# Performance work log

Measured on AMD Instinct MI355X. Metric: run time of the kernel, lower is better.

## Reference

```python
import jax, jax.numpy as jnp
import numpy as np

RADIUS = 4
SIGMA1 = 5.0
SIGMA2 = 1.0


def _gauss_1d(radius, sigma):
    x = jnp.arange(-radius, radius + 1, dtype=jnp.float32)
    return jnp.exp(-(x ** 2) / (2.0 * sigma ** 2))  # peak-1 gaussian (norm.pdf(d)/norm.pdf(0))


def _blur3d(x, g, radius):
    # Separable 3D gaussian conv; product of 1D kernels == exp(-(dx^2+dy^2+dz^2)/(2*sigma^2)),
    # mathematically identical to the dense (2r+1)^3 conv3d in the torch module.
    dn = ('NCDHW', 'OIDHW', 'NCDHW')
    for ax in range(3):
        shape = [1, 1, 1, 1, 1]
        shape[2 + ax] = g.shape[0]
        k = g.reshape(shape)
        pad = [(0, 0), (0, 0), (0, 0)]
        pad[ax] = (radius, radius)
        x = jax.lax.conv_general_dilated(x, k, (1, 1, 1), pad, dimension_numbers=dn)
    return x


def setup_inputs() -> dict:
    key = jax.random.key(0)
    k1, k2 = jax.random.split(key)
    labels = jax.random.uniform(k1, (2, 4, 128, 128, 128), dtype=jnp.float32)
    inputs = jax.random.normal(k2, (2, 1, 128, 128, 128), dtype=jnp.float32)
    return {"labels": labels, "inputs": inputs}


def reference(labels, inputs):
    num_classes = labels.shape[1]
    g = _gauss_1d(RADIUS, SIGMA1)
    loss = jnp.float32(0.0)
    for k in range(num_classes):
        class_probs = labels[:, k:k + 1]  # [B,1,D,H,W]
        class_mean = (jnp.mean(inputs * class_probs, axis=(2, 3, 4), keepdims=True)
                      / (jnp.mean(class_probs, axis=(2, 3, 4), keepdims=True) + 1e-5))  # [B,C,1,1,1]
        diff = jnp.sum((inputs - class_mean) ** 2, axis=1, keepdims=True)  # [B,1,D,H,W]
        weights = jnp.exp(-(diff ** 2) / (SIGMA2 ** 2))
        numerator = jnp.sum(class_probs * _blur3d(class_probs * weights, g, RADIUS))
        denominator = jnp.sum(class_probs * _blur3d(weights, g, RADIUS))
        # L1Loss(x, 0) on a scalar == |x|
        loss = loss + jnp.abs(numerator / (denominator + 1e-6))
    return num_classes - loss
```

## Files before the change

### kernel.cpp

```cpp
#include <hip/hip_runtime.h>
#include <math.h>

#define DIM   128
#define SLICE (DIM*DIM)
#define VOL   (DIM*DIM*DIM)
#define NK    4
#define NVOL  8
#define SSTR  33

__constant__ float c_g[9] = {
    0.72614904f, 0.83527021f, 0.92311635f, 0.98019867f, 1.0f,
    0.98019867f, 0.92311635f, 0.83527021f, 0.72614904f
};


__global__ __launch_bounds__(256) void k_sums(
    const float* __restrict__ labels, const float* __restrict__ inputs,
    float* __restrict__ red)
{
    const int b     = blockIdx.x >> 9;
    const int chunk = blockIdx.x & 511;
    const int t     = threadIdx.x;
    const size_t off4 = (size_t)chunk*1024 + t;
    const float4* __restrict__ I4 = (const float4*)inputs + (size_t)b*(VOL/4) + off4;
    const float4* __restrict__ L4 = (const float4*)labels;
    float sp[4] = {0,0,0,0}, sip[4] = {0,0,0,0};
    #pragma unroll
    for (int j = 0; j < 4; ++j) {
        const float4 iv = I4[j*256];
        #pragma unroll
        for (int k = 0; k < 4; ++k) {
            const float4 p = L4[(size_t)(b*NK + k)*(VOL/4) + off4 + j*256];
            sp[k]  += p.x + p.y + p.z + p.w;
            sip[k] += p.x*iv.x + p.y*iv.y + p.z*iv.z + p.w*iv.w;
        }
    }
    #pragma unroll
    for (int k = 0; k < 4; ++k) {
        #pragma unroll
        for (int o = 32; o; o >>= 1) {
            sp[k]  += __shfl_down(sp[k],  o);
            sip[k] += __shfl_down(sip[k], o);
        }
    }
    __shared__ float sB[8][4];
    const int wid = t >> 6;
    if ((t & 63) == 0) {
        #pragma unroll
        for (int k = 0; k < 4; ++k) { sB[k][wid] = sp[k]; sB[4+k][wid] = sip[k]; }
    }
    __syncthreads();
    if (t < 8) {
        const float v = sB[t][0] + sB[t][1] + sB[t][2] + sB[t][3];
        atomicAdd(&red[(t < 4 ? 0 : 8) + b*NK + (t & 3)], v);
    }
}

__global__ __launch_bounds__(256) void k_fused(
    const float* __restrict__ labels, const float* __restrict__ inputs,
    const float* __restrict__ red, float* __restrict__ nd)
{
    __shared__ float4 sW[2][16*SSTR + 8];
    __shared__ float sN[4], sD[4];

    const int dq    = blockIdx.x & 3;
    const int strip = (blockIdx.x >> 2) & 15;
    const int vol   = blockIdx.x >> 6;
    const int b = vol >> 2, kcls = vol & 3;
    const int d0 = dq * 32;
    const int t  = threadIdx.x;
    const float g1 = c_g[5], g2 = c_g[6], g3 = c_g[7], g4 = c_g[8];
    const float4 z4 = make_float4(0.f, 0.f, 0.f, 0.f);

    const float* __restrict__ src = labels + (size_t)vol*VOL;
    const float mean = red[8+vol] / (red[vol] + 20.97152f);

    const int r0 = t >> 5, c0 = t & 31;
    const int r1 = r0 + 8;
    const int ho = t >> 5, wq = t & 31;

    const int hA = strip*8 - 4 + r0;
    const int hB = strip*8 - 4 + r1;
    const bool vA = (unsigned)hA < 128u;
    const bool vB = (unsigned)hB < 128u;
    const float4* __restrict__ rowA = (const float4*)(src + (size_t)(vA ? hA : 0)*DIM);
    const float4* __restrict__ rowB = (const float4*)(src + (size_t)(vB ? hB : 0)*DIM);

    const size_t ob4 = (size_t)(strip*8 + ho)*(DIM/4) + wq;
    const float4* __restrict__ P4 = (const float4*)src + ob4;
    const float4* __restrict__ I4 = (const float4*)(inputs + (size_t)b*VOL) + ob4;

    float4 ring[9];
    #pragma unroll
    for (int i = 0; i < 9; ++i) ring[i] = z4;
    float numAcc = 0.f, denAcc = 0.f;

    auto ldA = [&](int s, float4& pv, float4& cv, float4& nx) {
        pv = cv = nx = z4;
        if (vA && (unsigned)s < 128u) {
            const float4* rp = rowA + (size_t)s*(SLICE/4);
            cv = rp[c0];
            if (c0 > 0)  pv = rp[c0-1];
            if (c0 < 31) nx = rp[c0+1];
        }
    };
    auto ldB = [&](int s, float4& pv, float4& cv, float4& nx) {
        pv = cv = nx = z4;
        if (vB && (unsigned)s < 128u) {
            const float4* rp = rowB + (size_t)s*(SLICE/4);
            cv = rp[c0];
            if (c0 > 0)  pv = rp[c0-1];
            if (c0 < 31) nx = rp[c0+1];
        }
    };

    float4 Apv, Acv, Anx, Bpv, Bcv, Bnx;
    ldA(d0-4, Apv, Acv, Anx);
    ldB(d0-4, Bpv, Bcv, Bnx);

    #pragma unroll 2
    for (int s = d0-4; s < d0+36; ++s) {
        const float4 apv=Apv, acv=Acv, anx=Anx, bpv=Bpv, bcv=Bcv, bnx=Bnx;
        ldA(s+1, Apv, Acv, Anx);
        ldB(s+1, Bpv, Bcv, Bnx);
        float4 pc = z4, ic = z4;
        const bool outStep = (s >= d0+4);
        if (outStep) {
            pc = P4[(size_t)(s-4)*(SLICE/4)];
            ic = I4[(size_t)(s-4)*(SLICE/4)];
        }
        const int buf = s & 1;
        {
            float4 o;
            o.x = acv.x + g1*(apv.w+acv.y) + g2*(apv.z+acv.z) + g3*(apv.y+acv.w) + g4*(apv.x+anx.x);
            o.y = acv.y + g1*(acv.x+acv.z) + g2*(apv.w+acv.w) + g3*(apv.z+anx.x) + g4*(apv.y+anx.y);
            o.z = acv.z + g1*(acv.y+acv.w) + g2*(acv.x+anx.x) + g3*(apv.w+anx.y) + g4*(apv.z+anx.z);
            o.w = acv.w + g1*(acv.z+anx.x) + g2*(acv.y+anx.y) + g3*(acv.x+anx.z) + g4*(apv.w+anx.w);
            sW[buf][r0*SSTR + c0] = o;
        }
        {
            float4 o;
            o.x = bcv.x + g1*(bpv.w+bcv.y) + g2*(bpv.z+bcv.z) + g3*(bpv.y+bcv.w) + g4*(bpv.x+bnx.x);
            o.y = bcv.y + g1*(bcv.x+bcv.z) + g2*(bpv.w+bcv.w) + g3*(bpv.z+bnx.x) + g4*(bpv.y+bnx.y);
            o.z = bcv.z + g1*(bcv.y+bcv.w) + g2*(bcv.x+bnx.x) + g3*(bpv.w+bnx.y) + g4*(bpv.z+bnx.z);
            o.w = bcv.w + g1*(bcv.z+bnx.x) + g2*(bcv.y+bnx.y) + g3*(bcv.x+bnx.z) + g4*(bpv.w+bnx.w);
            sW[buf][r1*SSTR + c0] = o;
        }
        __syncthreads();
        float4 acc = sW[buf][(ho+4)*SSTR + wq];
        #pragma unroll
        for (int dt = 1; dt <= 4; ++dt) {
            const float g = c_g[4+dt];
            const float4 u = sW[buf][(ho+4-dt)*SSTR + wq];
            const float4 v = sW[buf][(ho+4+dt)*SSTR + wq];
            acc.x += g*(u.x+v.x); acc.y += g*(u.y+v.y);
            acc.z += g*(u.z+v.z); acc.w += g*(u.w+v.w);
        }
        #pragma unroll
        for (int i = 0; i < 8; ++i) ring[i] = ring[i+1];
        ring[8] = acc;
        if (outStep) {
            float4 B = ring[4];
            #pragma unroll
            for (int dt = 1; dt <= 4; ++dt) {
                const float g = c_g[4+dt];
                B.x += g*(ring[4+dt].x + ring[4-dt].x);
                B.y += g*(ring[4+dt].y + ring[4-dt].y);
                B.z += g*(ring[4+dt].z + ring[4-dt].z);
                B.w += g*(ring[4+dt].w + ring[4-dt].w);
            }
            { float df = ic.x - mean; df *= df; const float bw = B.x * __expf(-df*df); numAcc += bw*pc.x; denAcc += bw; }
            { float df = ic.y - mean; df *= df; const float bw = B.y * __expf(-df*df); numAcc += bw*pc.y; denAcc += bw; }
            { float df = ic.z - mean; df *= df; const float bw = B.z * __expf(-df*df); numAcc += bw*pc.z; denAcc += bw; }
            { float df = ic.w - mean; df *= df; const float bw = B.w * __expf(-df*df); numAcc += bw*pc.w; denAcc += bw; }
        }
    }

    #pragma unroll
    for (int o = 32; o; o >>= 1) { numAcc += __shfl_down(numAcc, o); denAcc += __shfl_down(denAcc, o); }
    if ((t & 63) == 0) { sN[t >> 6] = numAcc; sD[t >> 6] = denAcc; }
    __syncthreads();
    if (t == 0) {
        atomicAdd(&nd[kcls],   sN[0]+sN[1]+sN[2]+sN[3]);
        atomicAdd(&nd[4+kcls], sD[0]+sD[1]+sD[2]+sD[3]);
    }
}

__global__ void k_final(const float* __restrict__ red, float* __restrict__ out)
{
    float loss = 0.f;
    #pragma unroll
    for (int k = 0; k < 4; ++k) loss += fabsf(red[16+k] / (red[20+k] + 1e-6f));
    out[0] = (float)NK - loss;
}

extern "C" void kernel_launch(void* const* d_in, const int* in_sizes, int n_in,
                              void* d_out, int out_size, void* d_ws, size_t ws_size,
                              hipStream_t stream)
{
    const float* labels = (const float*)d_in[0];
    const float* inputs = (const float*)d_in[1];
    float* out = (float*)d_out;
    float* red = (float*)d_ws;

    hipMemsetAsync(red, 0, 24*sizeof(float), stream);
    k_sums<<<2*512, 256, 0, stream>>>(labels, inputs, red);
    k_fused<<<NVOL*16*4, 256, 0, stream>>>(labels, inputs, red, red + 16);
    k_final<<<1, 1, 0, stream>>>(red, out);
}
```

Baseline: 183.5 us.

## Fold final reduction into fused kernel, unroll depth loop with rotating ring, pad atomics

Removes the separate single-thread final kernel. The last block to finish, detected through an atomic completion counter, now computes the loss. The depth loop is fully unrolled in groups of ten so the nine-slice ring buffer is indexed statically instead of shifted every step. The reduction slots are spread 32 floats apart to avoid atomic contention on shared cache lines, and launch bounds now request two blocks per SIMD. In exchange it adds a threadfence, a completion counter and larger code size, and it risks register pressure from the unroll.

```diff
diff --git a/kernel.cpp b/kernel.cpp
--- a/kernel.cpp
+++ b/kernel.cpp
@@ -5,8 +5,9 @@
 #define SLICE (DIM*DIM)
 #define VOL   (DIM*DIM*DIM)
 #define NK    4
-#define NVOL  8
 #define SSTR  33
+#define WSS   32
+#define DONE  24
 
 __constant__ float c_g[9] = {
     0.72614904f, 0.83527021f, 0.92311635f, 0.98019867f, 1.0f,
@@ -52,13 +53,13 @@
     __syncthreads();
     if (t < 8) {
         const float v = sB[t][0] + sB[t][1] + sB[t][2] + sB[t][3];
-        atomicAdd(&red[(t < 4 ? 0 : 8) + b*NK + (t & 3)], v);
+        atomicAdd(&red[((t < 4 ? 0 : 8) + b*NK + (t & 3))*WSS], v);
     }
 }
 
-__global__ __launch_bounds__(256) void k_fused(
+__global__ __launch_bounds__(256, 2) void k_fused(
     const float* __restrict__ labels, const float* __restrict__ inputs,
-    const float* __restrict__ red, float* __restrict__ nd)
+    float* __restrict__ red, float* __restrict__ out)
 {
     __shared__ float4 sW[2][16*SSTR + 8];
     __shared__ float sN[4], sD[4];
@@ -73,7 +74,7 @@
     const float4 z4 = make_float4(0.f, 0.f, 0.f, 0.f);
 
     const float* __restrict__ src = labels + (size_t)vol*VOL;
-    const float mean = red[8+vol] / (red[vol] + 20.97152f);
+    const float mean = red[(8+vol)*WSS] / (red[vol*WSS] + 20.97152f);
 
     const int r0 = t >> 5, c0 = t & 31;
     const int r1 = r0 + 8;
@@ -90,9 +91,7 @@
     const float4* __restrict__ P4 = (const float4*)src + ob4;
     const float4* __restrict__ I4 = (const float4*)(inputs + (size_t)b*VOL) + ob4;
 
-    float4 ring[9];
-    #pragma unroll
-    for (int i = 0; i < 9; ++i) ring[i] = z4;
+    float4 ring[10];
     float numAcc = 0.f, denAcc = 0.f;
 
     auto ldA = [&](int s, float4& pv, float4& cv, float4& nx) {
@@ -118,80 +117,90 @@
     ldA(d0-4, Apv, Acv, Anx);
     ldB(d0-4, Bpv, Bcv, Bnx);
 
-    #pragma unroll 2
-    for (int s = d0-4; s < d0+36; ++s) {
-        const float4 apv=Apv, acv=Acv, anx=Anx, bpv=Bpv, bcv=Bcv, bnx=Bnx;
-        ldA(s+1, Apv, Acv, Anx);
-        ldB(s+1, Bpv, Bcv, Bnx);
-        float4 pc = z4, ic = z4;
-        const bool outStep = (s >= d0+4);
-        if (outStep) {
-            pc = P4[(size_t)(s-4)*(SLICE/4)];
-            ic = I4[(size_t)(s-4)*(SLICE/4)];
-        }
-        const int buf = s & 1;
-        {
-            float4 o;
-            o.x = acv.x + g1*(apv.w+acv.y) + g2*(apv.z+acv.z) + g3*(apv.y+acv.w) + g4*(apv.x+anx.x);
-            o.y = acv.y + g1*(acv.x+acv.z) + g2*(apv.w+acv.w) + g3*(apv.z+anx.x) + g4*(apv.y+anx.y);
-            o.z = acv.z + g1*(acv.y+acv.w) + g2*(acv.x+anx.x) + g3*(apv.w+anx.y) + g4*(apv.z+anx.z);
-            o.w = acv.w + g1*(acv.z+anx.x) + g2*(acv.y+anx.y) + g3*(acv.x+anx.z) + g4*(apv.w+anx.w);
-            sW[buf][r0*SSTR + c0] = o;
-        }
-        {
-            float4 o;
-            o.x = bcv.x + g1*(bpv.w+bcv.y) + g2*(bpv.z+bcv.z) + g3*(bpv.y+bcv.w) + g4*(bpv.x+bnx.x);
-            o.y = bcv.y + g1*(bcv.x+bcv.z) + g2*(bpv.w+bcv.w) + g3*(bpv.z+bnx.x) + g4*(bpv.y+bnx.y);
-            o.z = bcv.z + g1*(bcv.y+bcv.w) + g2*(bcv.x+bnx.x) + g3*(bpv.w+bnx.y) + g4*(bpv.z+bnx.z);
-            o.w = bcv.w + g1*(bcv.z+bnx.x) + g2*(bcv.y+bnx.y) + g3*(bcv.x+bnx.z) + g4*(bpv.w+bnx.w);
-            sW[buf][r1*SSTR + c0] = o;
-        }
-        __syncthreads();
-        float4 acc = sW[buf][(ho+4)*SSTR + wq];
-        #pragma unroll
-        for (int dt = 1; dt <= 4; ++dt) {
-            const float g = c_g[4+dt];
-            const float4 u = sW[buf][(ho+4-dt)*SSTR + wq];
-            const float4 v = sW[buf][(ho+4+dt)*SSTR + wq];
-            acc.x += g*(u.x+v.x); acc.y += g*(u.y+v.y);
-            acc.z += g*(u.z+v.z); acc.w += g*(u.w+v.w);
-        }
-        #pragma unroll
-        for (int i = 0; i < 8; ++i) ring[i] = ring[i+1];
-        ring[8] = acc;
-        if (outStep) {
-            float4 B = ring[4];
-            #pragma unroll
-            for (int dt = 1; dt <= 4; ++dt) {
-                const float g = c_g[4+dt];
-                B.x += g*(ring[4+dt].x + ring[4-dt].x);
-                B.y += g*(ring[4+dt].y + ring[4-dt].y);
-                B.z += g*(ring[4+dt].z + ring[4-dt].z);
-                B.w += g*(ring[4+dt].w + ring[4-dt].w);
-            }
-            { float df = ic.x - mean; df *= df; const float bw = B.x * __expf(-df*df); numAcc += bw*pc.x; denAcc += bw; }
-            { float df = ic.y - mean; df *= df; const float bw = B.y * __expf(-df*df); numAcc += bw*pc.y; denAcc += bw; }
-            { float df = ic.z - mean; df *= df; const float bw = B.z * __expf(-df*df); numAcc += bw*pc.z; denAcc += bw; }
-            { float df = ic.w - mean; df *= df; const float bw = B.w * __expf(-df*df); numAcc += bw*pc.w; denAcc += bw; }
-        }
-    }
+#define BODY(J, OUT)                                                          \
+    {                                                                         \
+        const int s = sBase + (J);                                            \
+        const float4 apv=Apv, acv=Acv, anx=Anx, bpv=Bpv, bcv=Bcv, bnx=Bnx;    \
+        ldA(s+1, Apv, Acv, Anx);                                              \
+        ldB(s+1, Bpv, Bcv, Bnx);                                              \
+        float4 pc = z4, ic = z4;                                              \
+        if (OUT) {                                                            \
+            pc = P4[(size_t)(s-4)*(SLICE/4)];                                 \
+            ic = I4[(size_t)(s-4)*(SLICE/4)];                                 \
+        }                                                                     \
+        {                                                  \
+            float4 o;                                                         \
+            o.x = acv.x + g1*(apv.w+acv.y) + g2*(apv.z+acv.z) + g3*(apv.y+acv.w) + g4*(apv.x+anx.x); \
+            o.y = acv.y + g1*(acv.x+acv.z) + g2*(apv.w+acv.w) + g3*(apv.z+anx.x) + g4*(apv.y+anx.y); \
+            o.z = acv.z + g1*(acv.y+acv.w) + g2*(acv.x+anx.x) + g3*(apv.w+anx.y) + g4*(apv.z+anx.z); \
+            o.w = acv.w + g1*(acv.z+anx.x) + g2*(acv.y+anx.y) + g3*(acv.x+anx.z) + g4*(apv.w+anx.w); \
+            sW[(J)&1][r0*SSTR + c0] = o;                                      \
+        }                                                                     \
+        {                                                  \
+            float4 o;                                                         \
+            o.x = bcv.x + g1*(bpv.w+bcv.y) + g2*(bpv.z+bcv.z) + g3*(bpv.y+bcv.w) + g4*(bpv.x+bnx.x); \
+            o.y = bcv.y + g1*(bcv.x+bcv.z) + g2*(bpv.w+bcv.w) + g3*(bpv.z+bnx.x) + g4*(bpv.y+bnx.y); \
+            o.z = bcv.z + g1*(bcv.y+bcv.w) + g2*(bcv.x+bnx.x) + g3*(bpv.w+bnx.y) + g4*(bpv.z+bnx.z); \
+            o.w = bcv.w + g1*(bcv.z+bnx.x) + g2*(bcv.y+bnx.y) + g3*(bcv.x+bnx.z) + g4*(bpv.w+bnx.w); \
+            sW[(J)&1][r1*SSTR + c0] = o;                                      \
+        }                                                                     \
+        __syncthreads();                                                      \
+        float4 acc = sW[(J)&1][(ho+4)*SSTR + wq];                             \
+        _Pragma("unroll")                                                     \
+        for (int dt = 1; dt <= 4; ++dt) {                                     \
+            const float g = c_g[4+dt];                                        \
+            const float4 u = sW[(J)&1][(ho+4-dt)*SSTR + wq];                  \
+            const float4 v = sW[(J)&1][(ho+4+dt)*SSTR + wq];                  \
+            acc.x += g*(u.x+v.x); acc.y += g*(u.y+v.y);                       \
+            acc.z += g*(u.z+v.z); acc.w += g*(u.w+v.w);                       \
+        }                                                                     \
+        ring[(J)] = acc;                                                      \
+        if (OUT) {                                                            \
+            float4 B = ring[((J)+6) % 10];                                    \
+            _Pragma("unroll")                                                 \
+            for (int dt = 1; dt <= 4; ++dt) {                                 \
+                const float g = c_g[4+dt];                                    \
+                const float4 u = ring[((J)+6-dt) % 10];                       \
+                const float4 v = ring[((J)+6+dt) % 10];                       \
+                B.x += g*(u.x+v.x); B.y += g*(u.y+v.y);                       \
+                B.z += g*(u.z+v.z); B.w += g*(u.w+v.w);                       \
+            }                                                                 \
+            { float df = ic.x - mean; df *= df; const float bw = B.x * __expf(-df*df); numAcc += bw*pc.x; denAcc += bw; } \
+            { float df = ic.y - mean; df *= df; const float bw = B.y * __expf(-df*df); numAcc += bw*pc.y; denAcc += bw; } \
+            { float df = ic.z - mean; df *= df; const float bw = B.z * __expf(-df*df); numAcc += bw*pc.z; denAcc += bw; } \
+            { float df = ic.w - mean; df *= df; const float bw = B.w * __expf(-df*df); numAcc += bw*pc.w; denAcc += bw; } \
+        }                                                                     \
+    }
+
+    for (int ii = 0; ii < 40; ii += 10) {
+        const int  sBase = d0 - 4 + ii;
+        const bool tail  = (ii > 0);
+        BODY(0, tail) BODY(1, tail) BODY(2, tail) BODY(3, tail)
+        BODY(4, tail) BODY(5, tail) BODY(6, tail) BODY(7, tail)
+        BODY(8, true) BODY(9, true)
+    }
+#undef BODY
 
     #pragma unroll
     for (int o = 32; o; o >>= 1) { numAcc += __shfl_down(numAcc, o); denAcc += __shfl_down(denAcc, o); }
     if ((t & 63) == 0) { sN[t >> 6] = numAcc; sD[t >> 6] = denAcc; }
     __syncthreads();
     if (t == 0) {
-        atomicAdd(&nd[kcls],   sN[0]+sN[1]+sN[2]+sN[3]);
-        atomicAdd(&nd[4+kcls], sD[0]+sD[1]+sD[2]+sD[3]);
-    }
-}
-
-__global__ void k_final(const float* __restrict__ red, float* __restrict__ out)
-{
-    float loss = 0.f;
-    #pragma unroll
-    for (int k = 0; k < 4; ++k) loss += fabsf(red[16+k] / (red[20+k] + 1e-6f));
-    out[0] = (float)NK - loss;
+        atomicAdd(&red[(16+kcls)*WSS], sN[0]+sN[1]+sN[2]+sN[3]);
+        atomicAdd(&red[(20+kcls)*WSS], sD[0]+sD[1]+sD[2]+sD[3]);
+        __threadfence();
+        const unsigned old = atomicAdd((unsigned int*)&red[DONE*WSS], 1u);
+        if (old == 511u) {
+            float loss = 0.f;
+            #pragma unroll
+            for (int k = 0; k < 4; ++k) {
+                const float nu = atomicAdd(&red[(16+k)*WSS], 0.0f);
+                const float de = atomicAdd(&red[(20+k)*WSS], 0.0f);
+                loss += fabsf(nu / (de + 1e-6f));
+            }
+            out[0] = (float)NK - loss;
+        }
+    }
 }
 
 extern "C" void kernel_launch(void* const* d_in, const int* in_sizes, int n_in,
@@ -203,8 +212,7 @@
     float* out = (float*)d_out;
     float* red = (float*)d_ws;
 
-    hipMemsetAsync(red, 0, 24*sizeof(float), stream);
+    hipMemsetAsync(red, 0, 26*WSS*sizeof(float), stream);
     k_sums<<<2*512, 256, 0, stream>>>(labels, inputs, red);
-    k_fused<<<NVOL*16*4, 256, 0, stream>>>(labels, inputs, red, red + 16);
-    k_final<<<1, 1, 0, stream>>>(red, out);
+    k_fused<<<8*16*4, 256, 0, stream>>>(labels, inputs, red, out);
 }
```

After: 188.1 us. 2.5% more time.

## Fuse sums, blur and finalize into one kernel with per-volume spin barrier

Applied to the files above, without the earlier changes.

Merges the mean-reduction kernel, the fused blur kernel and the final scalar kernel into a single launch. Each block first reduces its own slab of labels and inputs, then waits on a per-volume atomic ticket counter (spinning with s_sleep) until all 64 blocks of that volume have contributed before computing the class mean. The last block to finish, found through a done counter, computes the loss, which replaces the separate finalize kernel. Counters are padded apart to reduce atomic contention. This removes two launches and the separate full read pass, but the design relies on all 512 blocks being co-resident to avoid deadlock and adds spin-wait latency.

```diff
diff --git a/kernel.cpp b/kernel.cpp
--- a/kernel.cpp
+++ b/kernel.cpp
@@ -5,8 +5,10 @@
 #define SLICE (DIM*DIM)
 #define VOL   (DIM*DIM*DIM)
 #define NK    4
-#define NVOL  8
 #define SSTR  33
+#define WSS   32
+#define DONE  24
+#define TICK  26
 
 __constant__ float c_g[9] = {
     0.72614904f, 0.83527021f, 0.92311635f, 0.98019867f, 1.0f,
@@ -14,54 +16,13 @@
 };
 
 
-__global__ __launch_bounds__(256) void k_sums(
+__global__ __launch_bounds__(256, 2) void k_all(
     const float* __restrict__ labels, const float* __restrict__ inputs,
-    float* __restrict__ red)
-{
-    const int b     = blockIdx.x >> 9;
-    const int chunk = blockIdx.x & 511;
-    const int t     = threadIdx.x;
-    const size_t off4 = (size_t)chunk*1024 + t;
-    const float4* __restrict__ I4 = (const float4*)inputs + (size_t)b*(VOL/4) + off4;
-    const float4* __restrict__ L4 = (const float4*)labels;
-    float sp[4] = {0,0,0,0}, sip[4] = {0,0,0,0};
-    #pragma unroll
-    for (int j = 0; j < 4; ++j) {
-        const float4 iv = I4[j*256];
-        #pragma unroll
-        for (int k = 0; k < 4; ++k) {
-            const float4 p = L4[(size_t)(b*NK + k)*(VOL/4) + off4 + j*256];
-            sp[k]  += p.x + p.y + p.z + p.w;
-            sip[k] += p.x*iv.x + p.y*iv.y + p.z*iv.z + p.w*iv.w;
-        }
-    }
-    #pragma unroll
-    for (int k = 0; k < 4; ++k) {
-        #pragma unroll
-        for (int o = 32; o; o >>= 1) {
-            sp[k]  += __shfl_down(sp[k],  o);
-            sip[k] += __shfl_down(sip[k], o);
-        }
-    }
-    __shared__ float sB[8][4];
-    const int wid = t >> 6;
-    if ((t & 63) == 0) {
-        #pragma unroll
-        for (int k = 0; k < 4; ++k) { sB[k][wid] = sp[k]; sB[4+k][wid] = sip[k]; }
-    }
-    __syncthreads();
-    if (t < 8) {
-        const float v = sB[t][0] + sB[t][1] + sB[t][2] + sB[t][3];
-        atomicAdd(&red[(t < 4 ? 0 : 8) + b*NK + (t & 3)], v);
-    }
-}
-
-__global__ __launch_bounds__(256) void k_fused(
-    const float* __restrict__ labels, const float* __restrict__ inputs,
-    const float* __restrict__ red, float* __restrict__ nd)
+    float* __restrict__ red, float* __restrict__ out)
 {
     __shared__ float4 sW[2][16*SSTR + 8];
     __shared__ float sN[4], sD[4];
+    __shared__ float sMean;
 
     const int dq    = blockIdx.x & 3;
     const int strip = (blockIdx.x >> 2) & 15;
@@ -72,8 +33,41 @@
     const float g1 = c_g[5], g2 = c_g[6], g3 = c_g[7], g4 = c_g[8];
     const float4 z4 = make_float4(0.f, 0.f, 0.f, 0.f);
 
+    {
+        const int rr = t >> 5, cc = t & 31;
+        const size_t roff = (size_t)d0*(SLICE/4) + (size_t)(strip*8)*(DIM/4)
+                          + (size_t)rr*(DIM/4) + cc;
+        const float4* __restrict__ Pa = (const float4*)labels + (size_t)vol*(VOL/4) + roff;
+        const float4* __restrict__ Ia = (const float4*)inputs + (size_t)b  *(VOL/4) + roff;
+        float sp = 0.f, sip = 0.f;
+        #pragma unroll 4
+        for (int s = 0; s < 32; ++s) {
+            const float4 p  = Pa[(size_t)s*(SLICE/4)];
+            const float4 iv = Ia[(size_t)s*(SLICE/4)];
+            sp  += p.x + p.y + p.z + p.w;
+            sip += p.x*iv.x + p.y*iv.y + p.z*iv.z + p.w*iv.w;
+        }
+        #pragma unroll
+        for (int o = 32; o; o >>= 1) { sp += __shfl_down(sp, o); sip += __shfl_down(sip, o); }
+        if ((t & 63) == 0) { sN[t >> 6] = sp; sD[t >> 6] = sip; }
+        __syncthreads();
+        if (t == 0) {
+            atomicAdd(&red[vol*WSS],     sN[0]+sN[1]+sN[2]+sN[3]);
+            atomicAdd(&red[(8+vol)*WSS], sD[0]+sD[1]+sD[2]+sD[3]);
+            __threadfence();
+            atomicAdd((unsigned int*)&red[(TICK+vol)*WSS], 1u);
+            while (__hip_atomic_load((unsigned int*)&red[(TICK+vol)*WSS],
+                                     __ATOMIC_ACQUIRE, __HIP_MEMORY_SCOPE_AGENT) < 64u)
+                __builtin_amdgcn_s_sleep(2);
+            const float sumP  = atomicAdd(&red[vol*WSS],     0.0f);
+            const float sumIP = atomicAdd(&red[(8+vol)*WSS], 0.0f);
+            sMean = sumIP / (sumP + 20.97152f);
+        }
+        __syncthreads();
+    }
+    const float mean = sMean;
+
     const float* __restrict__ src = labels + (size_t)vol*VOL;
-    const float mean = red[8+vol] / (red[vol] + 20.97152f);
 
     const int r0 = t >> 5, c0 = t & 31;
     const int r1 = r0 + 8;
@@ -181,17 +175,21 @@
     if ((t & 63) == 0) { sN[t >> 6] = numAcc; sD[t >> 6] = denAcc; }
     __syncthreads();
     if (t == 0) {
-        atomicAdd(&nd[kcls],   sN[0]+sN[1]+sN[2]+sN[3]);
-        atomicAdd(&nd[4+kcls], sD[0]+sD[1]+sD[2]+sD[3]);
+        atomicAdd(&red[(16+kcls)*WSS], sN[0]+sN[1]+sN[2]+sN[3]);
+        atomicAdd(&red[(20+kcls)*WSS], sD[0]+sD[1]+sD[2]+sD[3]);
+        __threadfence();
+        const unsigned old = atomicAdd((unsigned int*)&red[DONE*WSS], 1u);
+        if (old == 511u) {
+            float loss = 0.f;
+            #pragma unroll
+            for (int k = 0; k < 4; ++k) {
+                const float nu = atomicAdd(&red[(16+k)*WSS], 0.0f);
+                const float de = atomicAdd(&red[(20+k)*WSS], 0.0f);
+                loss += fabsf(nu / (de + 1e-6f));
+            }
+            out[0] = (float)NK - loss;
+        }
     }
-}
-
-__global__ void k_final(const float* __restrict__ red, float* __restrict__ out)
-{
-    float loss = 0.f;
-    #pragma unroll
-    for (int k = 0; k < 4; ++k) loss += fabsf(red[16+k] / (red[20+k] + 1e-6f));
-    out[0] = (float)NK - loss;
 }
 
 extern "C" void kernel_launch(void* const* d_in, const int* in_sizes, int n_in,
@@ -203,8 +201,6 @@
     float* out = (float*)d_out;
     float* red = (float*)d_ws;
 
-    hipMemsetAsync(red, 0, 24*sizeof(float), stream);
-    k_sums<<<2*512, 256, 0, stream>>>(labels, inputs, red);
-    k_fused<<<NVOL*16*4, 256, 0, stream>>>(labels, inputs, red, red + 16);
-    k_final<<<1, 1, 0, stream>>>(red, out);
+    hipMemsetAsync(red, 0, 34*WSS*sizeof(float), stream);
+    k_all<<<8*16*4, 256, 0, stream>>>(labels, inputs, red, out);
 }
```

Result: slower. 229.6 us (+25.1%).

## Split blur tile per wave, use wave barriers, fuse final reduction

Applied to the files above, without the earlier changes.

Each wavefront now owns an 8-column by 16-row strip of the per-slice H-blur tile in its own LDS region, so block-wide __syncthreads in the slice loop become wave-level barriers. It also drops the separate final kernel by having the last block, found through an atomic counter, compute the loss. It pads the reduction slots to separate cache lines and adds a launch-bounds occupancy hint. The risks are a narrower per-wave tile with more boundary loads, and correctness that depends on wave-synchronous LDS behaviour and the fence/atomic ordering.

```diff
diff --git a/kernel.cpp b/kernel.cpp
--- a/kernel.cpp
+++ b/kernel.cpp
@@ -5,8 +5,9 @@
 #define SLICE (DIM*DIM)
 #define VOL   (DIM*DIM*DIM)
 #define NK    4
-#define NVOL  8
-#define SSTR  33
+#define SW9   9
+#define WSS   32
+#define DONE  24
 
 __constant__ float c_g[9] = {
     0.72614904f, 0.83527021f, 0.92311635f, 0.98019867f, 1.0f,
@@ -52,15 +53,15 @@
     __syncthreads();
     if (t < 8) {
         const float v = sB[t][0] + sB[t][1] + sB[t][2] + sB[t][3];
-        atomicAdd(&red[(t < 4 ? 0 : 8) + b*NK + (t & 3)], v);
+        atomicAdd(&red[((t < 4 ? 0 : 8) + b*NK + (t & 3))*WSS], v);
     }
 }
 
-__global__ __launch_bounds__(256) void k_fused(
+__global__ __launch_bounds__(256, 2) void k_fused(
     const float* __restrict__ labels, const float* __restrict__ inputs,
-    const float* __restrict__ red, float* __restrict__ nd)
+    float* __restrict__ red, float* __restrict__ out)
 {
-    __shared__ float4 sW[2][16*SSTR + 8];
+    __shared__ float4 sWall[4][16*SW9];
     __shared__ float sN[4], sD[4];
 
     const int dq    = blockIdx.x & 3;
@@ -68,16 +69,21 @@
     const int vol   = blockIdx.x >> 6;
     const int b = vol >> 2, kcls = vol & 3;
     const int d0 = dq * 32;
-    const int t  = threadIdx.x;
+    const int t    = threadIdx.x;
+    const int wave = t >> 6, lane = t & 63;
     const float g1 = c_g[5], g2 = c_g[6], g3 = c_g[7], g4 = c_g[8];
     const float4 z4 = make_float4(0.f, 0.f, 0.f, 0.f);
 
+    float4* __restrict__ sWv = sWall[wave];
+
     const float* __restrict__ src = labels + (size_t)vol*VOL;
-    const float mean = red[8+vol] / (red[vol] + 20.97152f);
-
-    const int r0 = t >> 5, c0 = t & 31;
+    const float mean = red[(8+vol)*WSS] / (red[vol*WSS] + 20.97152f);
+
+    const int c0 = lane & 7, r0 = lane >> 3;
     const int r1 = r0 + 8;
-    const int ho = t >> 5, wq = t & 31;
+    const int gc = wave*8 + c0;
+    const int ho = lane >> 3, wqc = lane & 7;
+    const int gco = wave*8 + wqc;
 
     const int hA = strip*8 - 4 + r0;
     const int hB = strip*8 - 4 + r1;
@@ -86,7 +92,7 @@
     const float4* __restrict__ rowA = (const float4*)(src + (size_t)(vA ? hA : 0)*DIM);
     const float4* __restrict__ rowB = (const float4*)(src + (size_t)(vB ? hB : 0)*DIM);
 
-    const size_t ob4 = (size_t)(strip*8 + ho)*(DIM/4) + wq;
+    const size_t ob4 = (size_t)(strip*8 + ho)*(DIM/4) + gco;
     const float4* __restrict__ P4 = (const float4*)src + ob4;
     const float4* __restrict__ I4 = (const float4*)(inputs + (size_t)b*VOL) + ob4;
 
@@ -99,18 +105,18 @@
         pv = cv = nx = z4;
         if (vA && (unsigned)s < 128u) {
             const float4* rp = rowA + (size_t)s*(SLICE/4);
-            cv = rp[c0];
-            if (c0 > 0)  pv = rp[c0-1];
-            if (c0 < 31) nx = rp[c0+1];
+            cv = rp[gc];
+            if (gc > 0)  pv = rp[gc-1];
+            if (gc < 31) nx = rp[gc+1];
         }
     };
     auto ldB = [&](int s, float4& pv, float4& cv, float4& nx) {
         pv = cv = nx = z4;
         if (vB && (unsigned)s < 128u) {
             const float4* rp = rowB + (size_t)s*(SLICE/4);
-            cv = rp[c0];
-            if (c0 > 0)  pv = rp[c0-1];
-            if (c0 < 31) nx = rp[c0+1];
+            cv = rp[gc];
+            if (gc > 0)  pv = rp[gc-1];
+            if (gc < 31) nx = rp[gc+1];
         }
     };
 
@@ -129,14 +135,13 @@
             pc = P4[(size_t)(s-4)*(SLICE/4)];
             ic = I4[(size_t)(s-4)*(SLICE/4)];
         }
-        const int buf = s & 1;
         {
             float4 o;
             o.x = acv.x + g1*(apv.w+acv.y) + g2*(apv.z+acv.z) + g3*(apv.y+acv.w) + g4*(apv.x+anx.x);
             o.y = acv.y + g1*(acv.x+acv.z) + g2*(apv.w+acv.w) + g3*(apv.z+anx.x) + g4*(apv.y+anx.y);
             o.z = acv.z + g1*(acv.y+acv.w) + g2*(acv.x+anx.x) + g3*(apv.w+anx.y) + g4*(apv.z+anx.z);
             o.w = acv.w + g1*(acv.z+anx.x) + g2*(acv.y+anx.y) + g3*(acv.x+anx.z) + g4*(apv.w+anx.w);
-            sW[buf][r0*SSTR + c0] = o;
+            sWv[r0*SW9 + c0] = o;
         }
         {
             float4 o;
@@ -144,18 +149,19 @@
             o.y = bcv.y + g1*(bcv.x+bcv.z) + g2*(bpv.w+bcv.w) + g3*(bpv.z+bnx.x) + g4*(bpv.y+bnx.y);
             o.z = bcv.z + g1*(bcv.y+bcv.w) + g2*(bcv.x+bnx.x) + g3*(bpv.w+bnx.y) + g4*(bpv.z+bnx.z);
             o.w = bcv.w + g1*(bcv.z+bnx.x) + g2*(bcv.y+bnx.y) + g3*(bcv.x+bnx.z) + g4*(bpv.w+bnx.w);
-            sW[buf][r1*SSTR + c0] = o;
-        }
-        __syncthreads();
-        float4 acc = sW[buf][(ho+4)*SSTR + wq];
+            sWv[r1*SW9 + c0] = o;
+        }
+        __builtin_amdgcn_wave_barrier();
+        float4 acc = sWv[(ho+4)*SW9 + wqc];
         #pragma unroll
         for (int dt = 1; dt <= 4; ++dt) {
             const float g = c_g[4+dt];
-            const float4 u = sW[buf][(ho+4-dt)*SSTR + wq];
-            const float4 v = sW[buf][(ho+4+dt)*SSTR + wq];
+            const float4 u = sWv[(ho+4-dt)*SW9 + wqc];
+            const float4 v = sWv[(ho+4+dt)*SW9 + wqc];
             acc.x += g*(u.x+v.x); acc.y += g*(u.y+v.y);
             acc.z += g*(u.z+v.z); acc.w += g*(u.w+v.w);
         }
+        __builtin_amdgcn_wave_barrier();
         #pragma unroll
         for (int i = 0; i < 8; ++i) ring[i] = ring[i+1];
         ring[8] = acc;
@@ -178,20 +184,24 @@
 
     #pragma unroll
     for (int o = 32; o; o >>= 1) { numAcc += __shfl_down(numAcc, o); denAcc += __shfl_down(denAcc, o); }
-    if ((t & 63) == 0) { sN[t >> 6] = numAcc; sD[t >> 6] = denAcc; }
+    if (lane == 0) { sN[wave] = numAcc; sD[wave] = denAcc; }
     __syncthreads();
     if (t == 0) {
-        atomicAdd(&nd[kcls],   sN[0]+sN[1]+sN[2]+sN[3]);
-        atomicAdd(&nd[4+kcls], sD[0]+sD[1]+sD[2]+sD[3]);
-    }
-}
-
-__global__ void k_final(const float* __restrict__ red, float* __restrict__ out)
-{
-    float loss = 0.f;
-    #pragma unroll
-    for (int k = 0; k < 4; ++k) loss += fabsf(red[16+k] / (red[20+k] + 1e-6f));
-    out[0] = (float)NK - loss;
+        atomicAdd(&red[(16+kcls)*WSS], sN[0]+sN[1]+sN[2]+sN[3]);
+        atomicAdd(&red[(20+kcls)*WSS], sD[0]+sD[1]+sD[2]+sD[3]);
+        __threadfence();
+        const unsigned old = atomicAdd((unsigned int*)&red[DONE*WSS], 1u);
+        if (old == 511u) {
+            float loss = 0.f;
+            #pragma unroll
+            for (int k = 0; k < 4; ++k) {
+                const float nu = atomicAdd(&red[(16+k)*WSS], 0.0f);
+                const float de = atomicAdd(&red[(20+k)*WSS], 0.0f);
+                loss += fabsf(nu / (de + 1e-6f));
+            }
+            out[0] = (float)NK - loss;
+        }
+    }
 }
 
 extern "C" void kernel_launch(void* const* d_in, const int* in_sizes, int n_in,
@@ -203,8 +213,7 @@
     float* out = (float*)d_out;
     float* red = (float*)d_ws;
 
-    hipMemsetAsync(red, 0, 24*sizeof(float), stream);
+    hipMemsetAsync(red, 0, 25*WSS*sizeof(float), stream);
     k_sums<<<2*512, 256, 0, stream>>>(labels, inputs, red);
-    k_fused<<<NVOL*16*4, 256, 0, stream>>>(labels, inputs, red, red + 16);
-    k_final<<<1, 1, 0, stream>>>(red, out);
+    k_fused<<<8*16*4, 256, 0, stream>>>(labels, inputs, red, out);
 }
```

Measured after the change: 192.3 us. 1.05x slower.
